# Optimization experiments

Measured on AMD Instinct MI355X. Metric: run time of the kernel, lower is better.

Reference implementation:

```python
import jax, jax.numpy as jnp
import numpy as np

DIM = 128
HEADS = 4
DIM_HEAD = 32
HIDDEN = HEADS * DIM_HEAD  # 128
SCALE = DIM_HEAD ** -0.5


def setup_inputs() -> dict:
    key = jax.random.key(0)
    k1, k2, k3, k4 = jax.random.split(key, 4)
    b, c, h, w = 2, DIM, 64, 64
    x = jax.random.normal(k1, (b, c, h, w), dtype=jnp.float32)
    # conv1x1 weights stored as [out_ch, in_ch] (kernel is 1x1)
    w_qkv = jax.random.normal(k2, (3 * HIDDEN, DIM), dtype=jnp.float32) * (DIM ** -0.5)
    w_out = jax.random.normal(k3, (DIM, HIDDEN), dtype=jnp.float32) * (HIDDEN ** -0.5)
    b_out = jax.random.normal(k4, (DIM,), dtype=jnp.float32) * 0.01
    return {"x": x, "w_qkv": w_qkv, "w_out": w_out, "b_out": b_out}


def reference(x, w_qkv, w_out, b_out):
    b, c, h, w = x.shape
    n = h * w
    xf = x.reshape(b, c, n)                                   # [b,c,n]
    qkv = jnp.einsum('oc,bcn->bon', w_qkv, xf)                # conv1x1, no bias
    q, k, v = jnp.split(qkv, 3, axis=1)                       # each [b,hidden,n]
    q = q.reshape(b, HEADS, DIM_HEAD, n) * SCALE
    k = k.reshape(b, HEADS, DIM_HEAD, n)
    v = v.reshape(b, HEADS, DIM_HEAD, n)
    sim = jnp.einsum('bhdi,bhdj->bhij', q, k)                 # [b,h,n,n]
    attn = jax.nn.softmax(sim, axis=-1)
    out = jnp.einsum('bhij,bhdj->bhdi', attn, v)              # [b,h,d,n]
    out = out.reshape(b, HIDDEN, n)
    out = jnp.einsum('oc,bcn->bon', w_out, out) + b_out[None, :, None]
    return out.reshape(b, c, h, w) + x
```

## Files before the change

kernel.cpp:

```cpp
#include <hip/hip_runtime.h>
#include <hip/hip_bf16.h>

typedef __hip_bfloat16 bf16;
typedef float    f32x16 __attribute__((ext_vector_type(16)));
typedef __bf16   bf16x8 __attribute__((ext_vector_type(8)));
typedef unsigned uint4v __attribute__((ext_vector_type(4)));
typedef int      i32x2  __attribute__((ext_vector_type(2)));

#define N_TOK 4096
#define SCALE_L2E 0.2550348952703927f

__device__ __forceinline__ bf16x8 ld8(const bf16* p) { return *(const bf16x8*)p; }
__device__ __forceinline__ unsigned pack2(float a, float b) {
    unsigned short ua = __builtin_bit_cast(unsigned short, (__bf16)a);
    unsigned short ub = __builtin_bit_cast(unsigned short, (__bf16)b);
    return (unsigned)ua | ((unsigned)ub << 16);
}
__device__ __forceinline__ unsigned short f2b(float f) {
    return __builtin_bit_cast(unsigned short, (__bf16)f);
}
__device__ __forceinline__ __bf16 us2bf(unsigned short u) {
    return __builtin_bit_cast(__bf16, u);
}

__global__ void wconv(const float* __restrict__ wqkv, const float* __restrict__ wout,
                      bf16* __restrict__ wq, bf16* __restrict__ wo) {
    int idx = blockIdx.x * 256 + threadIdx.x;
    if (idx < 384 * 128) {
        float sc = (idx < 128 * 128) ? SCALE_L2E : 1.0f;
        ((unsigned short*)wq)[idx] = f2b(wqkv[idx] * sc);
    } else {
        int j = idx - 384 * 128;
        ((unsigned short*)wo)[j] = f2b(wout[j]);
    }
}

__global__ void __launch_bounds__(256)
qkv_mfma(const float* __restrict__ x, const bf16* __restrict__ wq,
         bf16* __restrict__ qt, bf16* __restrict__ kt, bf16* __restrict__ vt) {
    int tok0 = blockIdx.x * 32;
    int b    = blockIdx.y;
    __shared__ unsigned short xs[128][32];
    {
        int c = threadIdx.x >> 1, hf = threadIdx.x & 1;
        const float4* x4 = (const float4*)(x + (size_t)b * (128 * N_TOK) +
                                           (size_t)c * N_TOK + tok0 + hf * 16);
        float4 a = x4[0], bb = x4[1], cc = x4[2], dd = x4[3];
        unsigned* dst = (unsigned*)&xs[c][hf * 16];
        dst[0] = pack2(a.x, a.y);  dst[1] = pack2(a.z, a.w);
        dst[2] = pack2(bb.x, bb.y); dst[3] = pack2(bb.z, bb.w);
        dst[4] = pack2(cc.x, cc.y); dst[5] = pack2(cc.z, cc.w);
        dst[6] = pack2(dd.x, dd.y); dst[7] = pack2(dd.z, dd.w);
    }
    __syncthreads();
    int lane = threadIdx.x & 63, wv = threadIdx.x >> 6;
    int i = lane & 31, hl = lane >> 5;

    bf16x8 xf[8];
#pragma unroll
    for (int kb = 0; kb < 8; ++kb) {
        bf16x8 f;
#pragma unroll
        for (int e = 0; e < 8; ++e) f[e] = us2bf(xs[kb * 16 + hl * 8 + e][i]);
        xf[kb] = f;
    }

    f32x16 Z;
#pragma unroll
    for (int r = 0; r < 16; ++r) Z[r] = 0.f;

    {
        const bf16* wrow = wq + (size_t)(wv * 32 + i) * 128 + hl * 8;
        f32x16 D = Z;
#pragma unroll
        for (int kb = 0; kb < 8; ++kb)
            D = __builtin_amdgcn_mfma_f32_32x32x16_bf16(xf[kb], ld8(wrow + kb * 16), D, 0, 0, 0);
        unsigned short* dst = (unsigned short*)(qt + ((size_t)(b * 4 + wv) * N_TOK + tok0) * 32);
#pragma unroll
        for (int r = 0; r < 16; ++r) {
            int tr = (r & 3) + 8 * (r >> 2) + 4 * hl;
            dst[tr * 32 + i] = f2b(D[r]);
        }
    }
    {
        const bf16* wrow = wq + (size_t)(128 + wv * 32 + i) * 128 + hl * 8;
        f32x16 D = Z;
#pragma unroll
        for (int kb = 0; kb < 8; ++kb)
            D = __builtin_amdgcn_mfma_f32_32x32x16_bf16(xf[kb], ld8(wrow + kb * 16), D, 0, 0, 0);
        unsigned short* dst = (unsigned short*)(kt + ((size_t)(b * 4 + wv) * N_TOK + tok0) * 32);
#pragma unroll
        for (int r = 0; r < 16; ++r) {
            int tr = (r & 3) + 8 * (r >> 2) + 4 * hl;
            dst[tr * 32 + i] = f2b(D[r]);
        }
    }
    {
        const bf16* wrow = wq + (size_t)(256 + wv * 32 + i) * 128 + hl * 8;
        f32x16 D = Z;
#pragma unroll
        for (int kb = 0; kb < 8; ++kb)
            D = __builtin_amdgcn_mfma_f32_32x32x16_bf16(ld8(wrow + kb * 16), xf[kb], D, 0, 0, 0);
        unsigned short* dst = (unsigned short*)(vt + (size_t)(b * 4 + wv) * (32 * N_TOK) + tok0);
#pragma unroll
        for (int r = 0; r < 16; ++r) {
            int dr = (r & 3) + 8 * (r >> 2) + 4 * hl;
            dst[(size_t)dr * N_TOK + i] = f2b(D[r]);
        }
    }
}

__global__ void __launch_bounds__(512)
attn_mfma(const bf16* __restrict__ qt, const bf16* __restrict__ kt,
          const bf16* __restrict__ vt, bf16* __restrict__ ao) {
    int bid   = blockIdx.x;
    int swz   = (bid & 7) * 128 + (bid >> 3);
    int bh    = swz >> 7;
    int qtile = swz & 127;
    int lane  = threadIdx.x & 63;
    int wv    = threadIdx.x >> 6;
    int i     = lane & 31;
    int hl    = lane >> 5;

    const bf16* qb = qt + (size_t)bh * (N_TOK * 32) + (size_t)(qtile * 32) * 32;
    const bf16* kb = kt + (size_t)bh * (N_TOK * 32);
    const bf16* vb = vt + (size_t)bh * (32 * N_TOK);

    bf16x8 q1 = ld8(qb + i * 32 + hl * 8);
    bf16x8 q2 = ld8(qb + i * 32 + 16 + hl * 8);

    f32x16 O, Z;
#pragma unroll
    for (int r = 0; r < 16; ++r) { O[r] = 0.f; Z[r] = 0.f; }
    float l = 0.f;

    const bf16* kp0 = kb + ((size_t)(wv * 512) + i) * 32 + hl * 8;
    const bf16* vp0 = vb + (size_t)i * N_TOK + wv * 512 + hl * 8;

    bf16x8 ka1 = ld8(kp0);
    bf16x8 ka2 = ld8(kp0 + 16);
    bf16x8 va1 = ld8(vp0);
    bf16x8 va2 = ld8(vp0 + 16);

    for (int lj = 0; lj < 512; lj += 32) {
        int jn = (lj + 32) & 511;
        bf16x8 nk1 = ld8(kp0 + (size_t)jn * 32);
        bf16x8 nk2 = ld8(kp0 + (size_t)jn * 32 + 16);
        bf16x8 nv1 = ld8(vp0 + jn);
        bf16x8 nv2 = ld8(vp0 + jn + 16);

        f32x16 S = __builtin_amdgcn_mfma_f32_32x32x16_bf16(ka1, q1, Z, 0, 0, 0);
        S = __builtin_amdgcn_mfma_f32_32x32x16_bf16(ka2, q2, S, 0, 0, 0);

        float p[16];
#pragma unroll
        for (int r = 0; r < 16; ++r) { p[r] = __builtin_amdgcn_exp2f(S[r]); l += p[r]; }

        unsigned pk0 = pack2(p[0], p[1]),   pk1 = pack2(p[2], p[3]);
        unsigned pk2 = pack2(p[4], p[5]),   pk3 = pack2(p[6], p[7]);
        unsigned pk4 = pack2(p[8], p[9]),   pk5 = pack2(p[10], p[11]);
        unsigned pk6 = pack2(p[12], p[13]), pk7 = pack2(p[14], p[15]);

        i32x2 s1 = __builtin_amdgcn_permlane32_swap((int)pk0, (int)pk2, false, false);
        i32x2 s2 = __builtin_amdgcn_permlane32_swap((int)pk1, (int)pk3, false, false);
        i32x2 s3 = __builtin_amdgcn_permlane32_swap((int)pk4, (int)pk6, false, false);
        i32x2 s4 = __builtin_amdgcn_permlane32_swap((int)pk5, (int)pk7, false, false);

        uint4v B1 = {(unsigned)s1.x, (unsigned)s2.x, (unsigned)s1.y, (unsigned)s2.y};
        uint4v B2 = {(unsigned)s3.x, (unsigned)s4.x, (unsigned)s3.y, (unsigned)s4.y};

        O = __builtin_amdgcn_mfma_f32_32x32x16_bf16(va1, __builtin_bit_cast(bf16x8, B1), O, 0, 0, 0);
        O = __builtin_amdgcn_mfma_f32_32x32x16_bf16(va2, __builtin_bit_cast(bf16x8, B2), O, 0, 0, 0);

        ka1 = nk1; ka2 = nk2; va1 = nv1; va2 = nv2;
    }

    l += __shfl_xor(l, 32);

    __shared__ float osh[8][16][64];
    __shared__ float lsh[8][64];
#pragma unroll
    for (int r = 0; r < 16; ++r) osh[wv][r][lane] = O[r];
    lsh[wv][lane] = l;
    __syncthreads();
    float lt = 0.f;
#pragma unroll
    for (int s = 0; s < 8; ++s) lt += lsh[s][lane];
    float inv = 1.f / lt;
    unsigned short* aop = (unsigned short*)(ao + (size_t)bh * (32 * N_TOK) + qtile * 32);
#pragma unroll
    for (int r = 0; r < 2; ++r) {
        int rr = wv * 2 + r;
        float s = 0.f;
#pragma unroll
        for (int q = 0; q < 8; ++q) s += osh[q][rr][lane];
        int d = (rr & 3) + 8 * (rr >> 2) + 4 * hl;
        aop[(size_t)d * N_TOK + i] = f2b(s * inv);
    }
}

__global__ void __launch_bounds__(256)
out_mfma(const bf16* __restrict__ ao, const bf16* __restrict__ wo,
         const float* __restrict__ bias, const float* __restrict__ x,
         float* __restrict__ out) {
    int tok0 = blockIdx.x * 32;
    int b    = blockIdx.y;
    __shared__ unsigned short as_[128][32];
    {
        int c = threadIdx.x >> 1, hf = threadIdx.x & 1;
        const uint4v* src = (const uint4v*)(ao + (size_t)b * (128 * N_TOK) +
                                            (size_t)c * N_TOK + tok0 + hf * 16);
        uint4v v0 = src[0], v1 = src[1];
        uint4v* dst = (uint4v*)&as_[c][hf * 16];
        dst[0] = v0; dst[1] = v1;
    }
    __syncthreads();
    int lane = threadIdx.x & 63, wv = threadIdx.x >> 6;
    int i = lane & 31, hl = lane >> 5;

    bf16x8 af[8];
#pragma unroll
    for (int kb = 0; kb < 8; ++kb) {
        bf16x8 f;
#pragma unroll
        for (int e = 0; e < 8; ++e) f[e] = us2bf(as_[kb * 16 + hl * 8 + e][i]);
        af[kb] = f;
    }

    f32x16 D;
#pragma unroll
    for (int r = 0; r < 16; ++r) D[r] = 0.f;
    const bf16* wrow = wo + (size_t)(wv * 32 + i) * 128 + hl * 8;
#pragma unroll
    for (int kb = 0; kb < 8; ++kb)
        D = __builtin_amdgcn_mfma_f32_32x32x16_bf16(ld8(wrow + kb * 16), af[kb], D, 0, 0, 0);

#pragma unroll
    for (int r = 0; r < 16; ++r) {
        int o_r = wv * 32 + (r & 3) + 8 * (r >> 2) + 4 * hl;
        size_t idx = ((size_t)b * 128 + o_r) * N_TOK + tok0 + i;
        out[idx] = D[r] + bias[o_r] + x[idx];
    }
}

extern "C" void kernel_launch(void* const* d_in, const int* in_sizes, int n_in,
                              void* d_out, int out_size, void* d_ws, size_t ws_size,
                              hipStream_t stream) {
    const float* x     = (const float*)d_in[0];
    const float* w_qkv = (const float*)d_in[1];
    const float* w_out = (const float*)d_in[2];
    const float* b_out = (const float*)d_in[3];
    float* out = (float*)d_out;

    bf16* qt = (bf16*)d_ws;
    bf16* kt = qt + (size_t)8 * N_TOK * 32;
    bf16* vt = kt + (size_t)8 * N_TOK * 32;
    bf16* ao = vt + (size_t)8 * N_TOK * 32;
    bf16* wq = ao + (size_t)2 * 128 * N_TOK;
    bf16* wo = wq + (size_t)384 * 128;

    wconv    <<<dim3(256), 256, 0, stream>>>(w_qkv, w_out, wq, wo);
    qkv_mfma <<<dim3(128, 2), 256, 0, stream>>>(x, wq, qt, kt, vt);
    attn_mfma<<<dim3(1024), 512, 0, stream>>>(qt, kt, vt, ao);
    out_mfma <<<dim3(128, 2), 256, 0, stream>>>(ao, wo, b_out, x, out);
}
```

Before: 120.2 us.

## Fuse weight conversion into projections, deepen attention prefetch, compute row sums via MFMA

Removes the separate weight-conversion kernel: the QKV and output projection kernels now load fp32 weights, convert them to bf16 into padded shared memory, and read them from there. The QKV kernel gains a z grid dimension so each block computes only one of Q, K or V. In the attention kernel the main loop is fully unrolled with a three-deep register ring for K and V prefetch. The softmax denominator is now accumulated by an extra MFMA against a ones vector, replacing the scalar exp-sum. In exchange every projection block converts a full 128x128 weight matrix, the QKV kernel reloads x for each of Q, K and V, and the attention loop issues two extra MFMAs per step.

Measured after the change: 118.6 us. Within noise of the previous version (-1.4%).

```diff
diff --git a/kernel.cpp b/kernel.cpp
--- a/kernel.cpp
+++ b/kernel.cpp
@@ -22,85 +22,77 @@
 __device__ __forceinline__ __bf16 us2bf(unsigned short u) {
     return __builtin_bit_cast(__bf16, u);
 }
-
-__global__ void wconv(const float* __restrict__ wqkv, const float* __restrict__ wout,
-                      bf16* __restrict__ wq, bf16* __restrict__ wo) {
-    int idx = blockIdx.x * 256 + threadIdx.x;
-    if (idx < 384 * 128) {
-        float sc = (idx < 128 * 128) ? SCALE_L2E : 1.0f;
-        ((unsigned short*)wq)[idx] = f2b(wqkv[idx] * sc);
-    } else {
-        int j = idx - 384 * 128;
-        ((unsigned short*)wo)[j] = f2b(wout[j]);
-    }
+__device__ __forceinline__ bf16x8 ldw(const unsigned short* rowp) {
+    uint2 lo = *(const uint2*)rowp;
+    uint2 hi = *(const uint2*)(rowp + 4);
+    uint4v u = {lo.x, lo.y, hi.x, hi.y};
+    return __builtin_bit_cast(bf16x8, u);
 }
 
 __global__ void __launch_bounds__(256)
-qkv_mfma(const float* __restrict__ x, const bf16* __restrict__ wq,
+qkv_mfma(const float* __restrict__ x, const float* __restrict__ w,
          bf16* __restrict__ qt, bf16* __restrict__ kt, bf16* __restrict__ vt) {
     int tok0 = blockIdx.x * 32;
     int b    = blockIdx.y;
+    int z    = blockIdx.z;
     __shared__ unsigned short xs[128][32];
+    __shared__ unsigned short wl[128][132];
     {
         int c = threadIdx.x >> 1, hf = threadIdx.x & 1;
         const float4* x4 = (const float4*)(x + (size_t)b * (128 * N_TOK) +
                                            (size_t)c * N_TOK + tok0 + hf * 16);
         float4 a = x4[0], bb = x4[1], cc = x4[2], dd = x4[3];
         unsigned* dst = (unsigned*)&xs[c][hf * 16];
-        dst[0] = pack2(a.x, a.y);  dst[1] = pack2(a.z, a.w);
+        dst[0] = pack2(a.x, a.y);   dst[1] = pack2(a.z, a.w);
         dst[2] = pack2(bb.x, bb.y); dst[3] = pack2(bb.z, bb.w);
         dst[4] = pack2(cc.x, cc.y); dst[5] = pack2(cc.z, cc.w);
         dst[6] = pack2(dd.x, dd.y); dst[7] = pack2(dd.z, dd.w);
     }
+    {
+        float sc = (z == 0) ? SCALE_L2E : 1.0f;
+        const float4* wb4 = (const float4*)(w + (size_t)z * 128 * 128);
+#pragma unroll
+        for (int s = 0; s < 16; ++s) {
+            int i4 = threadIdx.x + s * 256;
+            int o  = i4 >> 5, c4 = (i4 & 31) * 4;
+            float4 wv4 = wb4[i4];
+            *(uint2*)&wl[o][c4] = make_uint2(pack2(wv4.x * sc, wv4.y * sc),
+                                             pack2(wv4.z * sc, wv4.w * sc));
+        }
+    }
     __syncthreads();
     int lane = threadIdx.x & 63, wv = threadIdx.x >> 6;
     int i = lane & 31, hl = lane >> 5;
 
-    bf16x8 xf[8];
+    bf16x8 xf[8], wf[8];
 #pragma unroll
     for (int kb = 0; kb < 8; ++kb) {
         bf16x8 f;
 #pragma unroll
         for (int e = 0; e < 8; ++e) f[e] = us2bf(xs[kb * 16 + hl * 8 + e][i]);
         xf[kb] = f;
-    }
-
-    f32x16 Z;
-#pragma unroll
-    for (int r = 0; r < 16; ++r) Z[r] = 0.f;
-
-    {
-        const bf16* wrow = wq + (size_t)(wv * 32 + i) * 128 + hl * 8;
-        f32x16 D = Z;
+        wf[kb] = ldw(&wl[wv * 32 + i][kb * 16 + hl * 8]);
+    }
+
+    f32x16 D;
+#pragma unroll
+    for (int r = 0; r < 16; ++r) D[r] = 0.f;
+
+    if (z < 2) {
 #pragma unroll
         for (int kb = 0; kb < 8; ++kb)
-            D = __builtin_amdgcn_mfma_f32_32x32x16_bf16(xf[kb], ld8(wrow + kb * 16), D, 0, 0, 0);
-        unsigned short* dst = (unsigned short*)(qt + ((size_t)(b * 4 + wv) * N_TOK + tok0) * 32);
+            D = __builtin_amdgcn_mfma_f32_32x32x16_bf16(xf[kb], wf[kb], D, 0, 0, 0);
+        bf16* base = (z == 0) ? qt : kt;
+        unsigned short* dst = (unsigned short*)(base + ((size_t)(b * 4 + wv) * N_TOK + tok0) * 32);
 #pragma unroll
         for (int r = 0; r < 16; ++r) {
             int tr = (r & 3) + 8 * (r >> 2) + 4 * hl;
             dst[tr * 32 + i] = f2b(D[r]);
         }
-    }
-    {
-        const bf16* wrow = wq + (size_t)(128 + wv * 32 + i) * 128 + hl * 8;
-        f32x16 D = Z;
+    } else {
 #pragma unroll
         for (int kb = 0; kb < 8; ++kb)
-            D = __builtin_amdgcn_mfma_f32_32x32x16_bf16(xf[kb], ld8(wrow + kb * 16), D, 0, 0, 0);
-        unsigned short* dst = (unsigned short*)(kt + ((size_t)(b * 4 + wv) * N_TOK + tok0) * 32);
-#pragma unroll
-        for (int r = 0; r < 16; ++r) {
-            int tr = (r & 3) + 8 * (r >> 2) + 4 * hl;
-            dst[tr * 32 + i] = f2b(D[r]);
-        }
-    }
-    {
-        const bf16* wrow = wq + (size_t)(256 + wv * 32 + i) * 128 + hl * 8;
-        f32x16 D = Z;
-#pragma unroll
-        for (int kb = 0; kb < 8; ++kb)
-            D = __builtin_amdgcn_mfma_f32_32x32x16_bf16(ld8(wrow + kb * 16), xf[kb], D, 0, 0, 0);
+            D = __builtin_amdgcn_mfma_f32_32x32x16_bf16(wf[kb], xf[kb], D, 0, 0, 0);
         unsigned short* dst = (unsigned short*)(vt + (size_t)(b * 4 + wv) * (32 * N_TOK) + tok0);
 #pragma unroll
         for (int r = 0; r < 16; ++r) {
@@ -123,38 +115,43 @@
     int hl    = lane >> 5;
 
     const bf16* qb = qt + (size_t)bh * (N_TOK * 32) + (size_t)(qtile * 32) * 32;
-    const bf16* kb = kt + (size_t)bh * (N_TOK * 32);
-    const bf16* vb = vt + (size_t)bh * (32 * N_TOK);
+    const bf16* kp0 = kt + (size_t)bh * (N_TOK * 32) + ((size_t)(wv * 512) + i) * 32 + hl * 8;
+    const bf16* vp0 = vt + (size_t)bh * (32 * N_TOK) + (size_t)i * N_TOK + wv * 512 + hl * 8;
 
     bf16x8 q1 = ld8(qb + i * 32 + hl * 8);
     bf16x8 q2 = ld8(qb + i * 32 + 16 + hl * 8);
 
-    f32x16 O, Z;
-#pragma unroll
-    for (int r = 0; r < 16; ++r) { O[r] = 0.f; Z[r] = 0.f; }
-    float l = 0.f;
-
-    const bf16* kp0 = kb + ((size_t)(wv * 512) + i) * 32 + hl * 8;
-    const bf16* vp0 = vb + (size_t)i * N_TOK + wv * 512 + hl * 8;
-
-    bf16x8 ka1 = ld8(kp0);
-    bf16x8 ka2 = ld8(kp0 + 16);
-    bf16x8 va1 = ld8(vp0);
-    bf16x8 va2 = ld8(vp0 + 16);
-
-    for (int lj = 0; lj < 512; lj += 32) {
-        int jn = (lj + 32) & 511;
-        bf16x8 nk1 = ld8(kp0 + (size_t)jn * 32);
-        bf16x8 nk2 = ld8(kp0 + (size_t)jn * 32 + 16);
-        bf16x8 nv1 = ld8(vp0 + jn);
-        bf16x8 nv2 = ld8(vp0 + jn + 16);
-
-        f32x16 S = __builtin_amdgcn_mfma_f32_32x32x16_bf16(ka1, q1, Z, 0, 0, 0);
-        S = __builtin_amdgcn_mfma_f32_32x32x16_bf16(ka2, q2, S, 0, 0, 0);
+    bf16x8 ones;
+#pragma unroll
+    for (int e = 0; e < 8; ++e) ones[e] = us2bf(0x3F80);
+
+    f32x16 O, Ol, Z;
+#pragma unroll
+    for (int r = 0; r < 16; ++r) { O[r] = 0.f; Ol[r] = 0.f; Z[r] = 0.f; }
+
+    bf16x8 kr1[3], kr2[3], vr1[3], vr2[3];
+#pragma unroll
+    for (int t = 0; t < 3; ++t) {
+        kr1[t] = ld8(kp0 + (size_t)(t * 32) * 32);
+        kr2[t] = ld8(kp0 + (size_t)(t * 32) * 32 + 16);
+        vr1[t] = ld8(vp0 + t * 32);
+        vr2[t] = ld8(vp0 + t * 32 + 16);
+    }
+
+#pragma unroll
+    for (int it = 0; it < 16; ++it) {
+        const int cur = it % 3;
+        const int jn  = (it * 32 + 96) & 511;
+
+        f32x16 S = __builtin_amdgcn_mfma_f32_32x32x16_bf16(kr1[cur], q1, Z, 0, 0, 0);
+        S = __builtin_amdgcn_mfma_f32_32x32x16_bf16(kr2[cur], q2, S, 0, 0, 0);
+
+        kr1[cur] = ld8(kp0 + (size_t)jn * 32);
+        kr2[cur] = ld8(kp0 + (size_t)jn * 32 + 16);
 
         float p[16];
 #pragma unroll
-        for (int r = 0; r < 16; ++r) { p[r] = __builtin_amdgcn_exp2f(S[r]); l += p[r]; }
+        for (int r = 0; r < 16; ++r) p[r] = __builtin_amdgcn_exp2f(S[r]);
 
         unsigned pk0 = pack2(p[0], p[1]),   pk1 = pack2(p[2], p[3]);
         unsigned pk2 = pack2(p[4], p[5]),   pk3 = pack2(p[6], p[7]);
@@ -166,22 +163,25 @@
         i32x2 s3 = __builtin_amdgcn_permlane32_swap((int)pk4, (int)pk6, false, false);
         i32x2 s4 = __builtin_amdgcn_permlane32_swap((int)pk5, (int)pk7, false, false);
 
-        uint4v B1 = {(unsigned)s1.x, (unsigned)s2.x, (unsigned)s1.y, (unsigned)s2.y};
-        uint4v B2 = {(unsigned)s3.x, (unsigned)s4.x, (unsigned)s3.y, (unsigned)s4.y};
-
-        O = __builtin_amdgcn_mfma_f32_32x32x16_bf16(va1, __builtin_bit_cast(bf16x8, B1), O, 0, 0, 0);
-        O = __builtin_amdgcn_mfma_f32_32x32x16_bf16(va2, __builtin_bit_cast(bf16x8, B2), O, 0, 0, 0);
-
-        ka1 = nk1; ka2 = nk2; va1 = nv1; va2 = nv2;
-    }
-
-    l += __shfl_xor(l, 32);
+        uint4v B1u = {(unsigned)s1.x, (unsigned)s2.x, (unsigned)s1.y, (unsigned)s2.y};
+        uint4v B2u = {(unsigned)s3.x, (unsigned)s4.x, (unsigned)s3.y, (unsigned)s4.y};
+        bf16x8 B1 = __builtin_bit_cast(bf16x8, B1u);
+        bf16x8 B2 = __builtin_bit_cast(bf16x8, B2u);
+
+        O  = __builtin_amdgcn_mfma_f32_32x32x16_bf16(vr1[cur], B1, O, 0, 0, 0);
+        O  = __builtin_amdgcn_mfma_f32_32x32x16_bf16(vr2[cur], B2, O, 0, 0, 0);
+        Ol = __builtin_amdgcn_mfma_f32_32x32x16_bf16(ones, B1, Ol, 0, 0, 0);
+        Ol = __builtin_amdgcn_mfma_f32_32x32x16_bf16(ones, B2, Ol, 0, 0, 0);
+
+        vr1[cur] = ld8(vp0 + jn);
+        vr2[cur] = ld8(vp0 + jn + 16);
+    }
 
     __shared__ float osh[8][16][64];
     __shared__ float lsh[8][64];
 #pragma unroll
     for (int r = 0; r < 16; ++r) osh[wv][r][lane] = O[r];
-    lsh[wv][lane] = l;
+    lsh[wv][lane] = Ol[0];
     __syncthreads();
     float lt = 0.f;
 #pragma unroll
@@ -200,12 +200,13 @@
 }
 
 __global__ void __launch_bounds__(256)
-out_mfma(const bf16* __restrict__ ao, const bf16* __restrict__ wo,
+out_mfma(const bf16* __restrict__ ao, const float* __restrict__ w,
          const float* __restrict__ bias, const float* __restrict__ x,
          float* __restrict__ out) {
     int tok0 = blockIdx.x * 32;
     int b    = blockIdx.y;
     __shared__ unsigned short as_[128][32];
+    __shared__ unsigned short wl[128][132];
     {
         int c = threadIdx.x >> 1, hf = threadIdx.x & 1;
         const uint4v* src = (const uint4v*)(ao + (size_t)b * (128 * N_TOK) +
@@ -214,26 +215,36 @@
         uint4v* dst = (uint4v*)&as_[c][hf * 16];
         dst[0] = v0; dst[1] = v1;
     }
+    {
+        const float4* wb4 = (const float4*)w;
+#pragma unroll
+        for (int s = 0; s < 16; ++s) {
+            int i4 = threadIdx.x + s * 256;
+            int o  = i4 >> 5, c4 = (i4 & 31) * 4;
+            float4 wv4 = wb4[i4];
+            *(uint2*)&wl[o][c4] = make_uint2(pack2(wv4.x, wv4.y), pack2(wv4.z, wv4.w));
+        }
+    }
     __syncthreads();
     int lane = threadIdx.x & 63, wv = threadIdx.x >> 6;
     int i = lane & 31, hl = lane >> 5;
 
-    bf16x8 af[8];
+    bf16x8 af[8], wf[8];
 #pragma unroll
     for (int kb = 0; kb < 8; ++kb) {
         bf16x8 f;
 #pragma unroll
         for (int e = 0; e < 8; ++e) f[e] = us2bf(as_[kb * 16 + hl * 8 + e][i]);
         af[kb] = f;
+        wf[kb] = ldw(&wl[wv * 32 + i][kb * 16 + hl * 8]);
     }
 
     f32x16 D;
 #pragma unroll
     for (int r = 0; r < 16; ++r) D[r] = 0.f;
-    const bf16* wrow = wo + (size_t)(wv * 32 + i) * 128 + hl * 8;
 #pragma unroll
     for (int kb = 0; kb < 8; ++kb)
-        D = __builtin_amdgcn_mfma_f32_32x32x16_bf16(ld8(wrow + kb * 16), af[kb], D, 0, 0, 0);
+        D = __builtin_amdgcn_mfma_f32_32x32x16_bf16(wf[kb], af[kb], D, 0, 0, 0);
 
 #pragma unroll
     for (int r = 0; r < 16; ++r) {
@@ -256,11 +267,8 @@
     bf16* kt = qt + (size_t)8 * N_TOK * 32;
     bf16* vt = kt + (size_t)8 * N_TOK * 32;
     bf16* ao = vt + (size_t)8 * N_TOK * 32;
-    bf16* wq = ao + (size_t)2 * 128 * N_TOK;
-    bf16* wo = wq + (size_t)384 * 128;
-
-    wconv    <<<dim3(256), 256, 0, stream>>>(w_qkv, w_out, wq, wo);
-    qkv_mfma <<<dim3(128, 2), 256, 0, stream>>>(x, wq, qt, kt, vt);
+
+    qkv_mfma <<<dim3(128, 2, 3), 256, 0, stream>>>(x, w_qkv, qt, kt, vt);
     attn_mfma<<<dim3(1024), 512, 0, stream>>>(qt, kt, vt, ao);
-    out_mfma <<<dim3(128, 2), 256, 0, stream>>>(ao, wo, b_out, x, out);
-}
+    out_mfma <<<dim3(128, 2), 256, 0, stream>>>(ao, w_out, b_out, x, out);
+}
```

## Stage K/V tiles in double-buffered LDS and share them across query tiles

Applied to the files above, without the earlier changes.

The attention kernel now gives each block 128 queries. The block cooperatively loads 128-key K/V chunks into double-buffered, swizzled shared memory, and each wave computes two 32-query tiles over a quarter of the keys, so K/V global traffic is amortised across more queries. The final reduction across the split key ranges goes through shared memory. The QKV and output projection kernels are retiled to 64 tokens per block with a z-dimension over output-channel groups, which spreads the work over more blocks. Trade-offs: there are now 256 attention blocks instead of 1024, which may reduce occupancy, and a barrier is added every iteration.

New measurement: 112.3 us. 6.5% less time.

```diff
diff --git a/kernel.cpp b/kernel.cpp
--- a/kernel.cpp
+++ b/kernel.cpp
@@ -38,70 +38,62 @@
 __global__ void __launch_bounds__(256)
 qkv_mfma(const float* __restrict__ x, const bf16* __restrict__ wq,
          bf16* __restrict__ qt, bf16* __restrict__ kt, bf16* __restrict__ vt) {
-    int tok0 = blockIdx.x * 32;
+    int tok0 = blockIdx.x * 64;
     int b    = blockIdx.y;
-    __shared__ unsigned short xs[128][32];
+    int z    = blockIdx.z;
+    __shared__ unsigned short xs[128 * 64];
     {
-        int c = threadIdx.x >> 1, hf = threadIdx.x & 1;
-        const float4* x4 = (const float4*)(x + (size_t)b * (128 * N_TOK) +
-                                           (size_t)c * N_TOK + tok0 + hf * 16);
-        float4 a = x4[0], bb = x4[1], cc = x4[2], dd = x4[3];
-        unsigned* dst = (unsigned*)&xs[c][hf * 16];
-        dst[0] = pack2(a.x, a.y);  dst[1] = pack2(a.z, a.w);
-        dst[2] = pack2(bb.x, bb.y); dst[3] = pack2(bb.z, bb.w);
-        dst[4] = pack2(cc.x, cc.y); dst[5] = pack2(cc.z, cc.w);
-        dst[6] = pack2(dd.x, dd.y); dst[7] = pack2(dd.z, dd.w);
+        int c = threadIdx.x >> 1, half = threadIdx.x & 1;
+        const float4* x4 = (const float4*)(x + (size_t)(b * 128 + c) * N_TOK + tok0 + half * 32);
+        unsigned* dst = (unsigned*)&xs[c * 64 + half * 32];
+#pragma unroll
+        for (int k = 0; k < 8; ++k) {
+            float4 v4 = x4[k];
+            dst[2 * k]     = pack2(v4.x, v4.y);
+            dst[2 * k + 1] = pack2(v4.z, v4.w);
+        }
     }
     __syncthreads();
     int lane = threadIdx.x & 63, wv = threadIdx.x >> 6;
+    int tc = wv & 1, oh = wv >> 1;
+    int ot = z * 2 + oh;
+    int o0 = ot * 32;
     int i = lane & 31, hl = lane >> 5;
 
-    bf16x8 xf[8];
+    bf16x8 xf[8], wf[8];
 #pragma unroll
     for (int kb = 0; kb < 8; ++kb) {
         bf16x8 f;
 #pragma unroll
-        for (int e = 0; e < 8; ++e) f[e] = us2bf(xs[kb * 16 + hl * 8 + e][i]);
+        for (int e = 0; e < 8; ++e) f[e] = us2bf(xs[(kb * 16 + hl * 8 + e) * 64 + tc * 32 + i]);
         xf[kb] = f;
-    }
-
-    f32x16 Z;
-#pragma unroll
-    for (int r = 0; r < 16; ++r) Z[r] = 0.f;
-
-    {
-        const bf16* wrow = wq + (size_t)(wv * 32 + i) * 128 + hl * 8;
-        f32x16 D = Z;
+        wf[kb] = ld8(wq + (size_t)(o0 + i) * 128 + kb * 16 + hl * 8);
+    }
+
+    f32x16 D;
+#pragma unroll
+    for (int r = 0; r < 16; ++r) D[r] = 0.f;
+
+    if (ot < 8) {
 #pragma unroll
         for (int kb = 0; kb < 8; ++kb)
-            D = __builtin_amdgcn_mfma_f32_32x32x16_bf16(xf[kb], ld8(wrow + kb * 16), D, 0, 0, 0);
-        unsigned short* dst = (unsigned short*)(qt + ((size_t)(b * 4 + wv) * N_TOK + tok0) * 32);
+            D = __builtin_amdgcn_mfma_f32_32x32x16_bf16(xf[kb], wf[kb], D, 0, 0, 0);
+        bf16* base = (ot < 4) ? qt : kt;
+        int h = ot & 3;
+        unsigned short* dst = (unsigned short*)(base +
+            ((size_t)(b * 4 + h) * N_TOK + tok0 + tc * 32) * 32);
 #pragma unroll
         for (int r = 0; r < 16; ++r) {
             int tr = (r & 3) + 8 * (r >> 2) + 4 * hl;
             dst[tr * 32 + i] = f2b(D[r]);
         }
-    }
-    {
-        const bf16* wrow = wq + (size_t)(128 + wv * 32 + i) * 128 + hl * 8;
-        f32x16 D = Z;
+    } else {
 #pragma unroll
         for (int kb = 0; kb < 8; ++kb)
-            D = __builtin_amdgcn_mfma_f32_32x32x16_bf16(xf[kb], ld8(wrow + kb * 16), D, 0, 0, 0);
-        unsigned short* dst = (unsigned short*)(kt + ((size_t)(b * 4 + wv) * N_TOK + tok0) * 32);
-#pragma unroll
-        for (int r = 0; r < 16; ++r) {
-            int tr = (r & 3) + 8 * (r >> 2) + 4 * hl;
-            dst[tr * 32 + i] = f2b(D[r]);
-        }
-    }
-    {
-        const bf16* wrow = wq + (size_t)(256 + wv * 32 + i) * 128 + hl * 8;
-        f32x16 D = Z;
-#pragma unroll
-        for (int kb = 0; kb < 8; ++kb)
-            D = __builtin_amdgcn_mfma_f32_32x32x16_bf16(ld8(wrow + kb * 16), xf[kb], D, 0, 0, 0);
-        unsigned short* dst = (unsigned short*)(vt + (size_t)(b * 4 + wv) * (32 * N_TOK) + tok0);
+            D = __builtin_amdgcn_mfma_f32_32x32x16_bf16(wf[kb], xf[kb], D, 0, 0, 0);
+        int h = ot - 8;
+        unsigned short* dst = (unsigned short*)(vt +
+            (size_t)(b * 4 + h) * (32 * N_TOK) + tok0 + tc * 32);
 #pragma unroll
         for (int r = 0; r < 16; ++r) {
             int dr = (r & 3) + 8 * (r >> 2) + 4 * hl;
@@ -110,92 +102,144 @@
     }
 }
 
+#define KROW 40
+#define KBUF_SZ (128 * KROW * 2)
+#define VBUF_OFF (2 * KBUF_SZ)
+#define VBUF_SZ (32 * 128 * 2)
+
 __global__ void __launch_bounds__(512)
 attn_mfma(const bf16* __restrict__ qt, const bf16* __restrict__ kt,
           const bf16* __restrict__ vt, bf16* __restrict__ ao) {
-    int bid   = blockIdx.x;
-    int swz   = (bid & 7) * 128 + (bid >> 3);
-    int bh    = swz >> 7;
-    int qtile = swz & 127;
-    int lane  = threadIdx.x & 63;
-    int wv    = threadIdx.x >> 6;
-    int i     = lane & 31;
-    int hl    = lane >> 5;
-
-    const bf16* qb = qt + (size_t)bh * (N_TOK * 32) + (size_t)(qtile * 32) * 32;
-    const bf16* kb = kt + (size_t)bh * (N_TOK * 32);
-    const bf16* vb = vt + (size_t)bh * (32 * N_TOK);
-
-    bf16x8 q1 = ld8(qb + i * 32 + hl * 8);
-    bf16x8 q2 = ld8(qb + i * 32 + 16 + hl * 8);
-
-    f32x16 O, Z;
-#pragma unroll
-    for (int r = 0; r < 16; ++r) { O[r] = 0.f; Z[r] = 0.f; }
-    float l = 0.f;
-
-    const bf16* kp0 = kb + ((size_t)(wv * 512) + i) * 32 + hl * 8;
-    const bf16* vp0 = vb + (size_t)i * N_TOK + wv * 512 + hl * 8;
-
-    bf16x8 ka1 = ld8(kp0);
-    bf16x8 ka2 = ld8(kp0 + 16);
-    bf16x8 va1 = ld8(vp0);
-    bf16x8 va2 = ld8(vp0 + 16);
-
-    for (int lj = 0; lj < 512; lj += 32) {
-        int jn = (lj + 32) & 511;
-        bf16x8 nk1 = ld8(kp0 + (size_t)jn * 32);
-        bf16x8 nk2 = ld8(kp0 + (size_t)jn * 32 + 16);
-        bf16x8 nv1 = ld8(vp0 + jn);
-        bf16x8 nv2 = ld8(vp0 + jn + 16);
-
-        f32x16 S = __builtin_amdgcn_mfma_f32_32x32x16_bf16(ka1, q1, Z, 0, 0, 0);
-        S = __builtin_amdgcn_mfma_f32_32x32x16_bf16(ka2, q2, S, 0, 0, 0);
-
-        float p[16];
-#pragma unroll
-        for (int r = 0; r < 16; ++r) { p[r] = __builtin_amdgcn_exp2f(S[r]); l += p[r]; }
-
-        unsigned pk0 = pack2(p[0], p[1]),   pk1 = pack2(p[2], p[3]);
-        unsigned pk2 = pack2(p[4], p[5]),   pk3 = pack2(p[6], p[7]);
-        unsigned pk4 = pack2(p[8], p[9]),   pk5 = pack2(p[10], p[11]);
-        unsigned pk6 = pack2(p[12], p[13]), pk7 = pack2(p[14], p[15]);
-
-        i32x2 s1 = __builtin_amdgcn_permlane32_swap((int)pk0, (int)pk2, false, false);
-        i32x2 s2 = __builtin_amdgcn_permlane32_swap((int)pk1, (int)pk3, false, false);
-        i32x2 s3 = __builtin_amdgcn_permlane32_swap((int)pk4, (int)pk6, false, false);
-        i32x2 s4 = __builtin_amdgcn_permlane32_swap((int)pk5, (int)pk7, false, false);
-
-        uint4v B1 = {(unsigned)s1.x, (unsigned)s2.x, (unsigned)s1.y, (unsigned)s2.y};
-        uint4v B2 = {(unsigned)s3.x, (unsigned)s4.x, (unsigned)s3.y, (unsigned)s4.y};
-
-        O = __builtin_amdgcn_mfma_f32_32x32x16_bf16(va1, __builtin_bit_cast(bf16x8, B1), O, 0, 0, 0);
-        O = __builtin_amdgcn_mfma_f32_32x32x16_bf16(va2, __builtin_bit_cast(bf16x8, B2), O, 0, 0, 0);
-
-        ka1 = nk1; ka2 = nk2; va1 = nv1; va2 = nv2;
-    }
-
-    l += __shfl_xor(l, 32);
-
-    __shared__ float osh[8][16][64];
-    __shared__ float lsh[8][64];
-#pragma unroll
-    for (int r = 0; r < 16; ++r) osh[wv][r][lane] = O[r];
-    lsh[wv][lane] = l;
+    int bid = blockIdx.x;
+    int bh  = bid & 7;
+    int qg  = bid >> 3;
+    int tid = threadIdx.x;
+    int lane = tid & 63, wv = tid >> 6;
+    int qp = wv >> 2;
+    int ks = wv & 3;
+    int i = lane & 31, hl = lane >> 5;
+
+    __shared__ char lds[2 * KBUF_SZ + 2 * VBUF_SZ];
+
+    const bf16* qb = qt + (size_t)bh * (N_TOK * 32) + (size_t)(qg * 128 + qp * 64) * 32;
+    bf16x8 q1a = ld8(qb + i * 32 + hl * 8);
+    bf16x8 q2a = ld8(qb + i * 32 + 16 + hl * 8);
+    bf16x8 q1b = ld8(qb + (32 + i) * 32 + hl * 8);
+    bf16x8 q2b = ld8(qb + (32 + i) * 32 + 16 + hl * 8);
+
+    int u = tid;
+    const bf16* ksrc = kt + (size_t)bh * (N_TOK * 32) + (u >> 2) * 32 + (u & 3) * 8;
+    const bf16* vsrc = vt + (size_t)bh * (32 * N_TOK) + (size_t)(u >> 4) * N_TOK + (u & 15) * 8;
+    int kdst = (u >> 2) * 80 + (u & 3) * 16;
+    int vdst = VBUF_OFF + (((u >> 4) * 256 + (u & 15) * 16) ^ (((u >> 4) & 7) << 4));
+
+    int koff1 = (ks * 32 + i) * 80 + hl * 16;
+    int koff2 = koff1 + 32;
+    int voff1 = VBUF_OFF + ((i * 256 + ks * 64 + hl * 16) ^ ((i & 7) << 4));
+    int voff2 = VBUF_OFF + ((i * 256 + ks * 64 + 32 + hl * 16) ^ ((i & 7) << 4));
+
+    f32x16 OA, OB, Z;
+#pragma unroll
+    for (int r = 0; r < 16; ++r) { OA[r] = 0.f; OB[r] = 0.f; Z[r] = 0.f; }
+    float lA = 0.f, lB = 0.f;
+
+    *(uint4v*)(lds + kdst) = *(const uint4v*)ksrc;
+    *(uint4v*)(lds + vdst) = *(const uint4v*)vsrc;
     __syncthreads();
-    float lt = 0.f;
-#pragma unroll
-    for (int s = 0; s < 8; ++s) lt += lsh[s][lane];
-    float inv = 1.f / lt;
-    unsigned short* aop = (unsigned short*)(ao + (size_t)bh * (32 * N_TOK) + qtile * 32);
-#pragma unroll
-    for (int r = 0; r < 2; ++r) {
-        int rr = wv * 2 + r;
-        float s = 0.f;
-#pragma unroll
-        for (int q = 0; q < 8; ++q) s += osh[q][rr][lane];
-        int d = (rr & 3) + 8 * (rr >> 2) + 4 * hl;
-        aop[(size_t)d * N_TOK + i] = f2b(s * inv);
+
+    for (int t = 0; t < 32; ++t) {
+        int cur = t & 1;
+        uint4v nk, nv;
+        if (t < 31) {
+            nk = *(const uint4v*)(ksrc + (size_t)(t + 1) * 128 * 32);
+            nv = *(const uint4v*)(vsrc + (t + 1) * 128);
+        }
+        bf16x8 ka1 = __builtin_bit_cast(bf16x8, *(const uint4v*)(lds + cur * KBUF_SZ + koff1));
+        bf16x8 ka2 = __builtin_bit_cast(bf16x8, *(const uint4v*)(lds + cur * KBUF_SZ + koff2));
+        bf16x8 va1 = __builtin_bit_cast(bf16x8, *(const uint4v*)(lds + cur * VBUF_SZ + voff1));
+        bf16x8 va2 = __builtin_bit_cast(bf16x8, *(const uint4v*)(lds + cur * VBUF_SZ + voff2));
+
+        f32x16 SA = __builtin_amdgcn_mfma_f32_32x32x16_bf16(ka1, q1a, Z, 0, 0, 0);
+        SA = __builtin_amdgcn_mfma_f32_32x32x16_bf16(ka2, q2a, SA, 0, 0, 0);
+        f32x16 SB = __builtin_amdgcn_mfma_f32_32x32x16_bf16(ka1, q1b, Z, 0, 0, 0);
+        SB = __builtin_amdgcn_mfma_f32_32x32x16_bf16(ka2, q2b, SB, 0, 0, 0);
+
+        float pA[16], pB[16];
+#pragma unroll
+        for (int r = 0; r < 16; ++r) { pA[r] = __builtin_amdgcn_exp2f(SA[r]); }
+#pragma unroll
+        for (int r = 0; r < 16; ++r) { pB[r] = __builtin_amdgcn_exp2f(SB[r]); }
+#pragma unroll
+        for (int r = 0; r < 16; ++r) { lA += pA[r]; lB += pB[r]; }
+
+        {
+            unsigned k0 = pack2(pA[0], pA[1]),   k1 = pack2(pA[2], pA[3]);
+            unsigned k2 = pack2(pA[4], pA[5]),   k3 = pack2(pA[6], pA[7]);
+            unsigned k4 = pack2(pA[8], pA[9]),   k5 = pack2(pA[10], pA[11]);
+            unsigned k6 = pack2(pA[12], pA[13]), k7 = pack2(pA[14], pA[15]);
+            i32x2 t1 = __builtin_amdgcn_permlane32_swap((int)k0, (int)k2, false, false);
+            i32x2 t2 = __builtin_amdgcn_permlane32_swap((int)k1, (int)k3, false, false);
+            i32x2 t3 = __builtin_amdgcn_permlane32_swap((int)k4, (int)k6, false, false);
+            i32x2 t4 = __builtin_amdgcn_permlane32_swap((int)k5, (int)k7, false, false);
+            uint4v B1u = {(unsigned)t1.x, (unsigned)t2.x, (unsigned)t1.y, (unsigned)t2.y};
+            uint4v B2u = {(unsigned)t3.x, (unsigned)t4.x, (unsigned)t3.y, (unsigned)t4.y};
+            OA = __builtin_amdgcn_mfma_f32_32x32x16_bf16(va1, __builtin_bit_cast(bf16x8, B1u), OA, 0, 0, 0);
+            OA = __builtin_amdgcn_mfma_f32_32x32x16_bf16(va2, __builtin_bit_cast(bf16x8, B2u), OA, 0, 0, 0);
+        }
+        {
+            unsigned k0 = pack2(pB[0], pB[1]),   k1 = pack2(pB[2], pB[3]);
+            unsigned k2 = pack2(pB[4], pB[5]),   k3 = pack2(pB[6], pB[7]);
+            unsigned k4 = pack2(pB[8], pB[9]),   k5 = pack2(pB[10], pB[11]);
+            unsigned k6 = pack2(pB[12], pB[13]), k7 = pack2(pB[14], pB[15]);
+            i32x2 t1 = __builtin_amdgcn_permlane32_swap((int)k0, (int)k2, false, false);
+            i32x2 t2 = __builtin_amdgcn_permlane32_swap((int)k1, (int)k3, false, false);
+            i32x2 t3 = __builtin_amdgcn_permlane32_swap((int)k4, (int)k6, false, false);
+            i32x2 t4 = __builtin_amdgcn_permlane32_swap((int)k5, (int)k7, false, false);
+            uint4v B1u = {(unsigned)t1.x, (unsigned)t2.x, (unsigned)t1.y, (unsigned)t2.y};
+            uint4v B2u = {(unsigned)t3.x, (unsigned)t4.x, (unsigned)t3.y, (unsigned)t4.y};
+            OB = __builtin_amdgcn_mfma_f32_32x32x16_bf16(va1, __builtin_bit_cast(bf16x8, B1u), OB, 0, 0, 0);
+            OB = __builtin_amdgcn_mfma_f32_32x32x16_bf16(va2, __builtin_bit_cast(bf16x8, B2u), OB, 0, 0, 0);
+        }
+
+        if (t < 31) {
+            int nxt = cur ^ 1;
+            *(uint4v*)(lds + nxt * KBUF_SZ + kdst) = nk;
+            *(uint4v*)(lds + nxt * VBUF_SZ + vdst) = nv;
+        }
+        __syncthreads();
+    }
+
+    lA += __shfl_xor(lA, 32);
+    lB += __shfl_xor(lB, 32);
+    float* fb = (float*)lds;
+    float* ls = (float*)(lds + 24576);
+    unsigned short* aop = (unsigned short*)(ao + (size_t)bh * (32 * N_TOK) + qg * 128 + qp * 64);
+
+#pragma unroll
+    for (int qtl = 0; qtl < 2; ++qtl) {
+        const f32x16& O = qtl ? OB : OA;
+        float l = qtl ? lB : lA;
+        if (ks) {
+            int s = qp * 3 + ks - 1;
+#pragma unroll
+            for (int r = 0; r < 16; ++r) fb[(s * 16 + r) * 64 + lane] = O[r];
+            ls[s * 64 + lane] = l;
+        }
+        __syncthreads();
+        if (ks == 0) {
+            int s0 = qp * 3;
+            float lt = l + ls[s0 * 64 + lane] + ls[(s0 + 1) * 64 + lane] + ls[(s0 + 2) * 64 + lane];
+            float inv = 1.f / lt;
+#pragma unroll
+            for (int r = 0; r < 16; ++r) {
+                float sv = O[r] + fb[((s0) * 16 + r) * 64 + lane] +
+                           fb[((s0 + 1) * 16 + r) * 64 + lane] +
+                           fb[((s0 + 2) * 16 + r) * 64 + lane];
+                int d = (r & 3) + 8 * (r >> 2) + 4 * hl;
+                aop[(size_t)d * N_TOK + qtl * 32 + i] = f2b(sv * inv);
+            }
+        }
+        __syncthreads();
     }
 }
 
@@ -203,42 +247,44 @@
 out_mfma(const bf16* __restrict__ ao, const bf16* __restrict__ wo,
          const float* __restrict__ bias, const float* __restrict__ x,
          float* __restrict__ out) {
-    int tok0 = blockIdx.x * 32;
+    int tok0 = blockIdx.x * 64;
     int b    = blockIdx.y;
-    __shared__ unsigned short as_[128][32];
+    int z    = blockIdx.z;
+    __shared__ unsigned short as_[128 * 64];
     {
-        int c = threadIdx.x >> 1, hf = threadIdx.x & 1;
-        const uint4v* src = (const uint4v*)(ao + (size_t)b * (128 * N_TOK) +
-                                            (size_t)c * N_TOK + tok0 + hf * 16);
-        uint4v v0 = src[0], v1 = src[1];
-        uint4v* dst = (uint4v*)&as_[c][hf * 16];
-        dst[0] = v0; dst[1] = v1;
+        int c = threadIdx.x >> 1, half = threadIdx.x & 1;
+        const uint4v* src = (const uint4v*)(ao + (size_t)(b * 128 + c) * N_TOK + tok0 + half * 32);
+        uint4v* dst = (uint4v*)&as_[c * 64 + half * 32];
+#pragma unroll
+        for (int k = 0; k < 4; ++k) dst[k] = src[k];
     }
     __syncthreads();
     int lane = threadIdx.x & 63, wv = threadIdx.x >> 6;
+    int tc = wv & 1, oh = wv >> 1;
+    int o0 = (z * 2 + oh) * 32;
     int i = lane & 31, hl = lane >> 5;
 
-    bf16x8 af[8];
+    bf16x8 af[8], wf[8];
 #pragma unroll
     for (int kb = 0; kb < 8; ++kb) {
         bf16x8 f;
 #pragma unroll
-        for (int e = 0; e < 8; ++e) f[e] = us2bf(as_[kb * 16 + hl * 8 + e][i]);
+        for (int e = 0; e < 8; ++e) f[e] = us2bf(as_[(kb * 16 + hl * 8 + e) * 64 + tc * 32 + i]);
         af[kb] = f;
+        wf[kb] = ld8(wo + (size_t)(o0 + i) * 128 + kb * 16 + hl * 8);
     }
 
     f32x16 D;
 #pragma unroll
     for (int r = 0; r < 16; ++r) D[r] = 0.f;
-    const bf16* wrow = wo + (size_t)(wv * 32 + i) * 128 + hl * 8;
 #pragma unroll
     for (int kb = 0; kb < 8; ++kb)
-        D = __builtin_amdgcn_mfma_f32_32x32x16_bf16(ld8(wrow + kb * 16), af[kb], D, 0, 0, 0);
+        D = __builtin_amdgcn_mfma_f32_32x32x16_bf16(wf[kb], af[kb], D, 0, 0, 0);
 
 #pragma unroll
     for (int r = 0; r < 16; ++r) {
-        int o_r = wv * 32 + (r & 3) + 8 * (r >> 2) + 4 * hl;
-        size_t idx = ((size_t)b * 128 + o_r) * N_TOK + tok0 + i;
+        int o_r = o0 + (r & 3) + 8 * (r >> 2) + 4 * hl;
+        size_t idx = ((size_t)b * 128 + o_r) * N_TOK + tok0 + tc * 32 + i;
         out[idx] = D[r] + bias[o_r] + x[idx];
     }
 }
@@ -260,7 +306,7 @@
     bf16* wo = wq + (size_t)384 * 128;
 
     wconv    <<<dim3(256), 256, 0, stream>>>(w_qkv, w_out, wq, wo);
-    qkv_mfma <<<dim3(128, 2), 256, 0, stream>>>(x, wq, qt, kt, vt);
-    attn_mfma<<<dim3(1024), 512, 0, stream>>>(qt, kt, vt, ao);
-    out_mfma <<<dim3(128, 2), 256, 0, stream>>>(ao, wo, b_out, x, out);
-}
+    qkv_mfma <<<dim3(64, 2, 6), 256, 0, stream>>>(x, wq, qt, kt, vt);
+    attn_mfma<<<dim3(256), 512, 0, stream>>>(qt, kt, vt, ao);
+    out_mfma <<<dim3(64, 2, 2), 256, 0, stream>>>(ao, wo, b_out, x, out);
+}
```
